# Optimization experiments

Hardware: AMD Instinct MI355X
Metric: run time of the kernel (lower is better)

Reference implementation:

```python
import jax, jax.numpy as jnp
import numpy as np

# Reconstructed from DAT's DAttentionBaseline with the wrapper's config:
# q_size=(14,14), n_heads=12, n_head_channels=64, n_groups=8, stride=1,
# offset_range_factor=1.0, use_pe=False (so log_cpb/rpe unused), no_off=False,
# ksize=3, dropout=0 (eval). Followed by the wrapper's Linear out-projection.

H = W = 14
G = 8          # n_groups
NH = 12        # n_heads
OFF_RANGE_FACTOR = 1.0


def grid_sample_bilinear(img, grid):
    # img: [B, C, H, W]; grid: [B, Hg, Wg, 2] in (x, y) order, [-1, 1],
    # align_corners=True, padding_mode='zeros' (torch defaults used by DAT).
    B, C, Hi, Wi = img.shape
    gx = (grid[..., 0] + 1.0) * 0.5 * (Wi - 1)
    gy = (grid[..., 1] + 1.0) * 0.5 * (Hi - 1)
    x0 = jnp.floor(gx)
    y0 = jnp.floor(gy)
    x1 = x0 + 1.0
    y1 = y0 + 1.0
    wx1 = gx - x0
    wx0 = 1.0 - wx1
    wy1 = gy - y0
    wy0 = 1.0 - wy1
    flat = img.reshape(B, C, Hi * Wi)

    def tap(xi, yi, wgt):
        valid = (xi >= 0) & (xi <= Wi - 1) & (yi >= 0) & (yi <= Hi - 1)
        xi_c = jnp.clip(xi, 0, Wi - 1).astype(jnp.int32)
        yi_c = jnp.clip(yi, 0, Hi - 1).astype(jnp.int32)
        idx = (yi_c * Wi + xi_c).reshape(B, 1, -1)
        vals = jnp.take_along_axis(flat, idx, axis=2)  # [B, C, Hg*Wg]
        w = (wgt * valid.astype(img.dtype)).reshape(B, 1, -1)
        return vals * w

    out = (tap(x0, y0, wx0 * wy0) + tap(x1, y0, wx1 * wy0)
           + tap(x0, y1, wx0 * wy1) + tap(x1, y1, wx1 * wy1))
    return out  # [B, C, Hg*Wg]


def setup_inputs() -> dict:
    key = jax.random.key(0)
    ks = jax.random.split(key, 16)
    B, N, C = 128, 196, 768
    Cg = C // G  # 96
    s = 0.02
    return {
        "hidden_states": jax.random.normal(ks[0], (B, N, C), jnp.float32),
        "Wq": jax.random.normal(ks[1], (C, C), jnp.float32) * s,
        "bq": jnp.zeros((C,), jnp.float32),
        "off_dw_w": jax.random.normal(ks[2], (Cg, 1, 3, 3), jnp.float32) * s,
        "off_dw_b": jnp.zeros((Cg,), jnp.float32),
        "ln_w": jnp.ones((Cg,), jnp.float32),
        "ln_b": jnp.zeros((Cg,), jnp.float32),
        "off_pw_w": jax.random.normal(ks[3], (2, Cg), jnp.float32) * s,
        "Wk": jax.random.normal(ks[4], (C, C), jnp.float32) * s,
        "bk": jnp.zeros((C,), jnp.float32),
        "Wv": jax.random.normal(ks[5], (C, C), jnp.float32) * s,
        "bv": jnp.zeros((C,), jnp.float32),
        "Wproj": jax.random.normal(ks[6], (C, C), jnp.float32) * s,
        "bproj": jnp.zeros((C,), jnp.float32),
        "Wout": jax.random.normal(ks[7], (C, C), jnp.float32) * s,
        "bout": jnp.zeros((C,), jnp.float32),
    }


def reference(hidden_states, Wq, bq, off_dw_w, off_dw_b, ln_w, ln_b, off_pw_w,
              Wk, bk, Wv, bv, Wproj, bproj, Wout, bout):
    B, N, C = hidden_states.shape
    Cg = C // G
    nh, dh = NH, C // NH
    scale = dh ** -0.5
    dt = hidden_states.dtype

    x_im = hidden_states.reshape(B, H, W, C).transpose(0, 3, 1, 2)  # [B,C,H,W]

    # proj_q: 1x1 conv
    q_im = jnp.einsum('bchw,oc->bohw', x_im, Wq) + bq[None, :, None, None]
    q_off = q_im.reshape(B * G, Cg, H, W)

    # offset net: depthwise 3x3 conv -> LayerNorm(channels) -> GELU -> 1x1 (no bias)
    t = jax.lax.conv_general_dilated(
        q_off, off_dw_w, (1, 1), [(1, 1), (1, 1)],
        dimension_numbers=('NCHW', 'OIHW', 'NCHW'), feature_group_count=Cg)
    t = t + off_dw_b[None, :, None, None]
    mu = t.mean(axis=1, keepdims=True)
    var = ((t - mu) ** 2).mean(axis=1, keepdims=True)
    t = (t - mu) * jax.lax.rsqrt(var + 1e-5)
    t = t * ln_w[None, :, None, None] + ln_b[None, :, None, None]
    t = jax.nn.gelu(t, approximate=False)
    off = jnp.einsum('bchw,oc->bohw', t, off_pw_w)  # [B*G, 2(y,x), H, W]

    off_range = jnp.array([1.0 / (H - 1), 1.0 / (W - 1)], dt).reshape(1, 2, 1, 1)
    off = jnp.tanh(off) * off_range * OFF_RANGE_FACTOR
    off = off.transpose(0, 2, 3, 1)  # [B*G, H, W, 2] (y, x)

    ry = ((jnp.arange(H, dtype=dt) + 0.5) / H) * 2.0 - 1.0
    rx = ((jnp.arange(W, dtype=dt) + 0.5) / W) * 2.0 - 1.0
    ref = jnp.stack(jnp.meshgrid(ry, rx, indexing='ij'), axis=-1)  # [H,W,2]
    pos = off + ref[None]          # (y, x)
    grid = pos[..., ::-1]          # (x, y) for grid_sample

    x_g = x_im.reshape(B * G, Cg, H, W)
    n_sample = H * W
    x_s = grid_sample_bilinear(x_g, grid).reshape(B, C, n_sample)

    k = jnp.einsum('bcn,oc->bon', x_s, Wk) + bk[None, :, None]
    v = jnp.einsum('bcn,oc->bon', x_s, Wv) + bv[None, :, None]

    qh = q_im.reshape(B, nh, dh, N)
    kh = k.reshape(B, nh, dh, n_sample)
    vh = v.reshape(B, nh, dh, n_sample)

    attn = jax.nn.softmax(jnp.einsum('bhcm,bhcn->bhmn', qh, kh) * scale, axis=-1)
    out = jnp.einsum('bhmn,bhcn->bhcm', attn, vh).reshape(B, C, N)

    y = jnp.einsum('bcn,oc->bon', out, Wproj) + bproj[None, :, None]
    y = y.transpose(0, 2, 1)               # [B, N, C]
    y = y @ Wout.T + bout                  # wrapper's Linear out-projection
    return y, attn
```

## Files before the change

### kernel.cpp

```cpp
#include <hip/hip_runtime.h>
#include <math.h>

#define Bsz 128
#define Hh 14
#define Ww 14
#define Nn 196
#define Cc 768
#define Gg 8
#define CgC 96
#define NHh 12
#define Dh 64
#define ROWS (Bsz*Nn)

typedef _Float16 half8 __attribute__((ext_vector_type(8)));
typedef _Float16 half4 __attribute__((ext_vector_type(4)));
typedef float f32x4 __attribute__((ext_vector_type(4)));

__global__ __launch_bounds__(256) void cvt_f32_f16(
    const float* __restrict__ src, _Float16* __restrict__ dst, int n8)
{
  const int i = blockIdx.x * 256 + threadIdx.x;
  if (i >= n8) return;
  float4 a = *(const float4*)(src + (size_t)i * 8);
  float4 b = *(const float4*)(src + (size_t)i * 8 + 4);
  half8 h;
  h[0]=(_Float16)a.x; h[1]=(_Float16)a.y; h[2]=(_Float16)a.z; h[3]=(_Float16)a.w;
  h[4]=(_Float16)b.x; h[5]=(_Float16)b.y; h[6]=(_Float16)b.z; h[7]=(_Float16)b.w;
  *(half8*)(dst + (size_t)i * 8) = h;
}

__global__ __launch_bounds__(256) void cvt_w5(
    const float* __restrict__ w0, const float* __restrict__ w1,
    const float* __restrict__ w2, const float* __restrict__ w3,
    const float* __restrict__ w4, _Float16* __restrict__ dst)
{
  const int i = blockIdx.x * 256 + threadIdx.x;
  const int per = Cc * Cc / 8;
  if (i >= 5 * per) return;
  const int m = i / per, r = i - m * per;
  const float* s = (m == 0) ? w0 : (m == 1) ? w1 : (m == 2) ? w2 : (m == 3) ? w3 : w4;
  float4 a = *(const float4*)(s + (size_t)r * 8);
  float4 b = *(const float4*)(s + (size_t)r * 8 + 4);
  half8 h;
  h[0]=(_Float16)a.x; h[1]=(_Float16)a.y; h[2]=(_Float16)a.z; h[3]=(_Float16)a.w;
  h[4]=(_Float16)b.x; h[5]=(_Float16)b.y; h[6]=(_Float16)b.z; h[7]=(_Float16)b.w;
  *(half8*)(dst + (size_t)m * Cc * Cc + (size_t)r * 8) = h;
}

template<int F16OUT>
__global__ __launch_bounds__(256) void gemm_h16(
    const _Float16* __restrict__ A, const _Float16* __restrict__ W,
    const float* __restrict__ bias, void* __restrict__ Cout)
{
  __shared__ __align__(16) _Float16 As[128 * 64];
  __shared__ __align__(16) _Float16 Bs[128 * 64];
  const int t = threadIdx.x;
  const int nwg = gridDim.x;
  int bid = blockIdx.x;
  bid = (bid & 7) * (nwg >> 3) + (bid >> 3);
  const int colb = bid % 6, rowb = bid / 6;
  const int row0 = rowb * 128, col0 = colb * 128;
  const int lane = t & 63, w = t >> 6;
  const int wr = w >> 1, wc = w & 1;
  const int l15 = lane & 15, l4 = lane >> 4;
  const int srow = t >> 3;
  const int sg   = t & 7;

  f32x4 acc[4][4];
#pragma unroll
  for (int i = 0; i < 4; ++i)
#pragma unroll
    for (int j = 0; j < 4; ++j) acc[i][j] = (f32x4){0.f, 0.f, 0.f, 0.f};

  for (int kt = 0; kt < 12; ++kt) {
    const int k0 = kt * 64;
#pragma unroll
    for (int it = 0; it < 4; ++it) {
      const int r = it * 32 + srow;
      half8 ha = *(const half8*)(A + (size_t)(row0 + r) * Cc + k0 + sg * 8);
      half8 hw = *(const half8*)(W + (size_t)(col0 + r) * Cc + k0 + sg * 8);
      const int dst = r * 64 + ((sg ^ (r & 7)) * 8);
      *(half8*)&As[dst] = ha;
      *(half8*)&Bs[dst] = hw;
    }
    __syncthreads();
#pragma unroll
    for (int ks = 0; ks < 2; ++ks) {
      half8 af[4], bf[4];
#pragma unroll
      for (int mi = 0; mi < 4; ++mi) {
        const int r = wr * 64 + mi * 16 + l15;
        const int g = ks * 4 + l4;
        af[mi] = *(const half8*)&As[r * 64 + ((g ^ (r & 7)) * 8)];
      }
#pragma unroll
      for (int ni = 0; ni < 4; ++ni) {
        const int r = wc * 64 + ni * 16 + l15;
        const int g = ks * 4 + l4;
        bf[ni] = *(const half8*)&Bs[r * 64 + ((g ^ (r & 7)) * 8)];
      }
#pragma unroll
      for (int mi = 0; mi < 4; ++mi)
#pragma unroll
        for (int ni = 0; ni < 4; ++ni)
          acc[mi][ni] = __builtin_amdgcn_mfma_f32_16x16x32_f16(af[mi], bf[ni], acc[mi][ni], 0, 0, 0);
    }
    __syncthreads();
  }

#pragma unroll
  for (int ni = 0; ni < 4; ++ni) {
    const int col = col0 + wc * 64 + ni * 16 + l15;
    const float bcol = bias[col];
#pragma unroll
    for (int mi = 0; mi < 4; ++mi) {
      f32x4 v = acc[mi][ni];
      const int rbase = row0 + wr * 64 + mi * 16 + l4 * 4;
#pragma unroll
      for (int r = 0; r < 4; ++r) {
        if (F16OUT) {
          ((_Float16*)Cout)[(size_t)(rbase + r) * Cc + col] = (_Float16)(v[r] + bcol);
        } else {
          ((float*)Cout)[(size_t)(rbase + r) * Cc + col] = v[r] + bcol;
        }
      }
    }
  }
}

__global__ __launch_bounds__(256) void gemm_h16_kv(
    const _Float16* __restrict__ A, const _Float16* __restrict__ Wkv,
    const float* __restrict__ bk, const float* __restrict__ bv,
    _Float16* __restrict__ K16, _Float16* __restrict__ V16)
{
  __shared__ __align__(16) _Float16 As[128 * 64];
  __shared__ __align__(16) _Float16 Bs[128 * 64];
  const int t = threadIdx.x;
  const int nwg = gridDim.x;
  int bid = blockIdx.x;
  bid = (bid & 7) * (nwg >> 3) + (bid >> 3);
  const int colb = bid % 12, rowb = bid / 12;
  const int row0 = rowb * 128, col0 = colb * 128;
  const int lane = t & 63, w = t >> 6;
  const int wr = w >> 1, wc = w & 1;
  const int l15 = lane & 15, l4 = lane >> 4;
  const int srow = t >> 3;
  const int sg   = t & 7;

  _Float16* Cout = (colb < 6) ? K16 : V16;
  const float* bias = (colb < 6) ? bk : bv;
  const int cadj = (colb < 6) ? 0 : Cc;

  f32x4 acc[4][4];
#pragma unroll
  for (int i = 0; i < 4; ++i)
#pragma unroll
    for (int j = 0; j < 4; ++j) acc[i][j] = (f32x4){0.f, 0.f, 0.f, 0.f};

  for (int kt = 0; kt < 12; ++kt) {
    const int k0 = kt * 64;
#pragma unroll
    for (int it = 0; it < 4; ++it) {
      const int r = it * 32 + srow;
      half8 ha = *(const half8*)(A + (size_t)(row0 + r) * Cc + k0 + sg * 8);
      half8 hw = *(const half8*)(Wkv + (size_t)(col0 + r) * Cc + k0 + sg * 8);
      const int dst = r * 64 + ((sg ^ (r & 7)) * 8);
      *(half8*)&As[dst] = ha;
      *(half8*)&Bs[dst] = hw;
    }
    __syncthreads();
#pragma unroll
    for (int ks = 0; ks < 2; ++ks) {
      half8 af[4], bf[4];
#pragma unroll
      for (int mi = 0; mi < 4; ++mi) {
        const int r = wr * 64 + mi * 16 + l15;
        const int g = ks * 4 + l4;
        af[mi] = *(const half8*)&As[r * 64 + ((g ^ (r & 7)) * 8)];
      }
#pragma unroll
      for (int ni = 0; ni < 4; ++ni) {
        const int r = wc * 64 + ni * 16 + l15;
        const int g = ks * 4 + l4;
        bf[ni] = *(const half8*)&Bs[r * 64 + ((g ^ (r & 7)) * 8)];
      }
#pragma unroll
      for (int mi = 0; mi < 4; ++mi)
#pragma unroll
        for (int ni = 0; ni < 4; ++ni)
          acc[mi][ni] = __builtin_amdgcn_mfma_f32_16x16x32_f16(af[mi], bf[ni], acc[mi][ni], 0, 0, 0);
    }
    __syncthreads();
  }

#pragma unroll
  for (int ni = 0; ni < 4; ++ni) {
    const int col = col0 + wc * 64 + ni * 16 + l15;
    const float bcol = bias[col - cadj];
#pragma unroll
    for (int mi = 0; mi < 4; ++mi) {
      f32x4 v = acc[mi][ni];
      const int rbase = row0 + wr * 64 + mi * 16 + l4 * 4;
#pragma unroll
      for (int r = 0; r < 4; ++r)
        Cout[(size_t)(rbase + r) * Cc + (col - cadj)] = (_Float16)(v[r] + bcol);
    }
  }
}

__global__ __launch_bounds__(512, 4) void offset_sample(
    const _Float16* __restrict__ Q16, const float* __restrict__ hidden,
    const float* __restrict__ dw_w, const float* __restrict__ dw_b,
    const float* __restrict__ ln_w, const float* __restrict__ ln_b,
    const float* __restrict__ pw_w, _Float16* __restrict__ XS)
{
  __shared__ float Qs[Nn * CgC];
  const int tid = threadIdx.x;
  const int g = blockIdx.x;
  const int b = blockIdx.y;
  const int cl = tid & 31;
  const int grp = tid >> 5;

  const size_t base = (size_t)b * Nn * Cc + g * CgC;
  for (int i = tid; i < Nn * 12; i += 512) {
    const int n = i / 12, j = i - n * 12;
    half8 hv = *(const half8*)(Q16 + base + (size_t)n * Cc + j * 8);
#pragma unroll
    for (int e = 0; e < 8; ++e) Qs[n * CgC + j * 8 + e] = (float)hv[e];
  }

  float wdw[3][9], bdw[3], wln[3], bln[3], wp0[3], wp1[3];
#pragma unroll
  for (int k = 0; k < 3; ++k) {
    const int c = cl + k * 32;
#pragma unroll
    for (int t9 = 0; t9 < 9; ++t9) wdw[k][t9] = dw_w[c * 9 + t9];
    bdw[k] = dw_b[c];
    wln[k] = ln_w[c];
    bln[k] = ln_b[c];
    wp0[k] = pw_w[c];
    wp1[k] = pw_w[CgC + c];
  }
  __syncthreads();

  const float* hb0 = hidden + base;

  for (int s0 = 0; s0 < Nn; s0 += 16) {
    const int site = s0 + grp;
    if (site >= Nn) break;
    const int h = site / Ww, w = site % Ww;

    float t[3];
#pragma unroll
    for (int k = 0; k < 3; ++k) t[k] = bdw[k];
#pragma unroll
    for (int ky = 0; ky < 3; ++ky) {
      const int hp = h + ky - 1;
      if (hp < 0 || hp > Hh - 1) continue;
#pragma unroll
      for (int kx = 0; kx < 3; ++kx) {
        const int wp = w + kx - 1;
        if (wp < 0 || wp > Ww - 1) continue;
        const float* row = &Qs[(hp * Ww + wp) * CgC + cl];
#pragma unroll
        for (int k = 0; k < 3; ++k)
          t[k] = fmaf(row[k * 32], wdw[k][ky * 3 + kx], t[k]);
      }
    }

    float s = t[0] + t[1] + t[2];
#pragma unroll
    for (int off = 1; off <= 16; off <<= 1) s += __shfl_xor(s, off, 32);
    const float mu = s * (1.f / 96.f);
    float d2 = 0.f;
#pragma unroll
    for (int k = 0; k < 3; ++k) { const float d = t[k] - mu; d2 = fmaf(d, d, d2); }
#pragma unroll
    for (int off = 1; off <= 16; off <<= 1) d2 += __shfl_xor(d2, off, 32);
    const float rstd = rsqrtf(d2 * (1.f / 96.f) + 1e-5f);

    float p0 = 0.f, p1 = 0.f;
#pragma unroll
    for (int k = 0; k < 3; ++k) {
      const float tn = (t[k] - mu) * rstd * wln[k] + bln[k];
      const float a = 0.5f * tn * (1.f + erff(tn * 0.70710678118654752f));
      p0 = fmaf(a, wp0[k], p0);
      p1 = fmaf(a, wp1[k], p1);
    }
#pragma unroll
    for (int off = 1; off <= 16; off <<= 1) {
      p0 += __shfl_xor(p0, off, 32);
      p1 += __shfl_xor(p1, off, 32);
    }

    const float offy = tanhf(p0) * (1.f / 13.f);
    const float offx = tanhf(p1) * (1.f / 13.f);
    const float refy = (h + 0.5f) / 14.f * 2.f - 1.f;
    const float refx = (w + 0.5f) / 14.f * 2.f - 1.f;
    const float gx = ((offx + refx) + 1.f) * 0.5f * 13.f;
    const float gy = ((offy + refy) + 1.f) * 0.5f * 13.f;

    const float x0f = floorf(gx), y0f = floorf(gy);
    const int x0 = (int)x0f, y0 = (int)y0f;
    const float wx1 = gx - x0f, wx0 = 1.f - wx1;
    const float wy1 = gy - y0f, wy0 = 1.f - wy1;
    const bool vx0 = (x0 >= 0) & (x0 <= 13), vx1 = (x0 + 1 >= 0) & (x0 + 1 <= 13);
    const bool vy0 = (y0 >= 0) & (y0 <= 13), vy1 = (y0 + 1 >= 0) & (y0 + 1 <= 13);
    float acc[3] = {0.f, 0.f, 0.f};
#pragma unroll
    for (int k = 0; k < 3; ++k) {
      const int c = cl + k * 32;
      if (vx0 & vy0) acc[k] = fmaf(wx0 * wy0, hb0[(size_t)(y0 * Ww + x0) * Cc + c], acc[k]);
      if (vx1 & vy0) acc[k] = fmaf(wx1 * wy0, hb0[(size_t)(y0 * Ww + x0 + 1) * Cc + c], acc[k]);
      if (vx0 & vy1) acc[k] = fmaf(wx0 * wy1, hb0[(size_t)((y0 + 1) * Ww + x0) * Cc + c], acc[k]);
      if (vx1 & vy1) acc[k] = fmaf(wx1 * wy1, hb0[(size_t)((y0 + 1) * Ww + x0 + 1) * Cc + c], acc[k]);
    }
    _Float16* xp = XS + ((size_t)b * Nn + site) * Cc + g * CgC + cl;
#pragma unroll
    for (int k = 0; k < 3; ++k) xp[k * 32] = (_Float16)acc[k];
  }
}

__global__ __launch_bounds__(512, 4) void attn_fused(
    const _Float16* __restrict__ Qm, const _Float16* __restrict__ Km,
    const _Float16* __restrict__ Vm, float* __restrict__ attn,
    _Float16* __restrict__ OUT)
{
  __shared__ __align__(16) _Float16 Kt[208 * 72];
  __shared__ __align__(16) _Float16 Vt[64 * 232];
  __shared__ __align__(16) _Float16 Ps[8][16 * 40];
  const int tid = threadIdx.x;
  const int hh = blockIdx.x, b = blockIdx.y;
  const int lane = tid & 63, wv = tid >> 6;
  const int l15 = lane & 15, l4 = lane >> 4;

  const _Float16* Qbase = Qm + (size_t)b * Nn * Cc + hh * Dh;
  const _Float16* Kbase = Km + (size_t)b * Nn * Cc + hh * Dh;
  const _Float16* Vbase = Vm + (size_t)b * Nn * Cc + hh * Dh;

  {
    const int g = tid & 7;
    for (int n = tid >> 3; n < 208; n += 64) {
      half8 hv = {};
      if (n < Nn) hv = *(const half8*)(Kbase + (size_t)n * Cc + g * 8);
      *(half8*)&Kt[n * 72 + g * 8] = hv;
    }
  }
  {
    const int d0 = (tid & 15) * 4;
    for (int n = tid >> 4; n < Nn; n += 32) {
      half4 v = *(const half4*)(Vbase + (size_t)n * Cc + d0);
      Vt[(d0 + 0) * 232 + n] = v[0];
      Vt[(d0 + 1) * 232 + n] = v[1];
      Vt[(d0 + 2) * 232 + n] = v[2];
      Vt[(d0 + 3) * 232 + n] = v[3];
    }
    for (int e = tid; e < 64 * 36; e += 512) {
      int d = e / 36, n = Nn + e % 36;
      Vt[d * 232 + n] = (_Float16)0.f;
    }
  }
  __syncthreads();

  for (int mt = wv; mt < 13; mt += 8) {
    const int qrow = mt * 16 + l15;
    const _Float16* qp = Qbase + (size_t)(qrow < Nn ? qrow : (Nn - 1)) * Cc + l4 * 8;
    half8 aq0 = *(const half8*)qp;
    half8 aq1 = *(const half8*)(qp + 32);

    f32x4 accs[13];
#pragma unroll
    for (int nt = 0; nt < 13; ++nt) accs[nt] = (f32x4){0.f, 0.f, 0.f, 0.f};
#pragma unroll
    for (int nt = 0; nt < 13; ++nt) {
      const int rb = (nt * 16 + l15) * 72;
      half8 bk0 = *(const half8*)&Kt[rb + l4 * 8];
      half8 bk1 = *(const half8*)&Kt[rb + 32 + l4 * 8];
      accs[nt] = __builtin_amdgcn_mfma_f32_16x16x32_f16(aq0, bk0, accs[nt], 0, 0, 0);
      accs[nt] = __builtin_amdgcn_mfma_f32_16x16x32_f16(aq1, bk1, accs[nt], 0, 0, 0);
    }

    float rmax[4] = {-1e30f, -1e30f, -1e30f, -1e30f};
#pragma unroll
    for (int nt = 0; nt < 13; ++nt) {
#pragma unroll
      for (int r = 0; r < 4; ++r) {
        float s = accs[nt][r] * 0.125f;
        if (nt == 12 && l15 >= 4) s = -1e30f;
        accs[nt][r] = s;
        rmax[r] = fmaxf(rmax[r], s);
      }
    }
#pragma unroll
    for (int off = 1; off <= 8; off <<= 1)
#pragma unroll
      for (int r = 0; r < 4; ++r)
        rmax[r] = fmaxf(rmax[r], __shfl_xor(rmax[r], off, 64));

    float rsum[4] = {0.f, 0.f, 0.f, 0.f};
#pragma unroll
    for (int nt = 0; nt < 13; ++nt) {
#pragma unroll
      for (int r = 0; r < 4; ++r) {
        float p = __expf(accs[nt][r] - rmax[r]);
        accs[nt][r] = p;
        rsum[r] += p;
      }
    }
#pragma unroll
    for (int off = 1; off <= 8; off <<= 1)
#pragma unroll
      for (int r = 0; r < 4; ++r)
        rsum[r] += __shfl_xor(rsum[r], off, 64);
    float rinv[4];
#pragma unroll
    for (int r = 0; r < 4; ++r) rinv[r] = 1.f / rsum[r];

    float* ab = attn + (((size_t)b * NHh + hh) * Nn) * (size_t)Nn;
#pragma unroll
    for (int nt = 0; nt < 13; ++nt) {
      const int n = nt * 16 + l15;
#pragma unroll
      for (int r = 0; r < 4; ++r) {
        float pr = accs[nt][r] * rinv[r];
        accs[nt][r] = pr;
        const int m = mt * 16 + l4 * 4 + r;
        if (m < Nn && n < Nn) ab[(size_t)m * Nn + n] = pr;
      }
    }

    f32x4 acco[4];
#pragma unroll
    for (int dt = 0; dt < 4; ++dt) acco[dt] = (f32x4){0.f, 0.f, 0.f, 0.f};
#pragma unroll
    for (int nsl = 0; nsl < 7; ++nsl) {
#pragma unroll
      for (int h2 = 0; h2 < 2; ++h2) {
        const int nt = nsl * 2 + h2;
        if (nt < 13) {
#pragma unroll
          for (int r = 0; r < 4; ++r)
            Ps[wv][(l4 * 4 + r) * 40 + h2 * 16 + l15] = (_Float16)accs[nt][r];
        } else {
#pragma unroll
          for (int r = 0; r < 4; ++r)
            Ps[wv][(l4 * 4 + r) * 40 + h2 * 16 + l15] = (_Float16)0.f;
        }
      }
      half8 ap = *(const half8*)&Ps[wv][l15 * 40 + l4 * 8];
#pragma unroll
      for (int dt = 0; dt < 4; ++dt) {
        half8 bv = *(const half8*)&Vt[(dt * 16 + l15) * 232 + nsl * 32 + l4 * 8];
        acco[dt] = __builtin_amdgcn_mfma_f32_16x16x32_f16(ap, bv, acco[dt], 0, 0, 0);
      }
    }
#pragma unroll
    for (int dt = 0; dt < 4; ++dt) {
#pragma unroll
      for (int r = 0; r < 4; ++r) {
        const int m = mt * 16 + l4 * 4 + r;
        if (m < Nn)
          OUT[((size_t)b * Nn + m) * Cc + hh * Dh + dt * 16 + l15] = (_Float16)acco[dt][r];
      }
    }
  }
}

extern "C" void kernel_launch(void* const* d_in, const int* in_sizes, int n_in,
                              void* d_out, int out_size, void* d_ws, size_t ws_size,
                              hipStream_t stream) {
  const float* hidden = (const float*)d_in[0];
  const float* Wq = (const float*)d_in[1];
  const float* bq = (const float*)d_in[2];
  const float* dw_w = (const float*)d_in[3];
  const float* dw_b = (const float*)d_in[4];
  const float* ln_w = (const float*)d_in[5];
  const float* ln_b = (const float*)d_in[6];
  const float* pw_w = (const float*)d_in[7];
  const float* Wk = (const float*)d_in[8];
  const float* bk = (const float*)d_in[9];
  const float* Wv = (const float*)d_in[10];
  const float* bv = (const float*)d_in[11];
  const float* Wp = (const float*)d_in[12];
  const float* bp = (const float*)d_in[13];
  const float* Wo = (const float*)d_in[14];
  const float* bo = (const float*)d_in[15];

  const size_t SZ = (size_t)Bsz * Nn * Cc;
  float* yout = (float*)d_out;
  float* attn = yout + SZ;

  _Float16* h16   = (_Float16*)d_ws;
  _Float16* Q16   = h16   + SZ;
  _Float16* XS16  = Q16   + SZ;
  _Float16* K16   = XS16  + SZ;
  _Float16* V16   = K16   + SZ;
  _Float16* OUT16 = V16   + SZ;
  _Float16* Y116  = OUT16 + SZ;
  _Float16* W16   = Y116  + SZ;

  const int gemm_blocks = (ROWS / 128) * (Cc / 128);
  const int kv_blocks   = (ROWS / 128) * 12;
  const int n8 = (int)(SZ / 8);

  cvt_f32_f16<<<(n8 + 255) / 256, 256, 0, stream>>>(hidden, h16, n8);
  cvt_w5<<<(5 * Cc * Cc / 8 + 255) / 256, 256, 0, stream>>>(Wq, Wk, Wv, Wp, Wo, W16);

  gemm_h16<1><<<gemm_blocks, 256, 0, stream>>>(h16, W16 + 0 * (size_t)Cc * Cc, bq, Q16);
  offset_sample<<<dim3(Gg, Bsz), 512, 0, stream>>>(Q16, hidden, dw_w, dw_b, ln_w, ln_b, pw_w, XS16);
  gemm_h16_kv<<<kv_blocks, 256, 0, stream>>>(XS16, W16 + 1 * (size_t)Cc * Cc, bk, bv, K16, V16);
  attn_fused<<<dim3(NHh, Bsz), 512, 0, stream>>>(Q16, K16, V16, attn, OUT16);
  gemm_h16<1><<<gemm_blocks, 256, 0, stream>>>(OUT16, W16 + 3 * (size_t)Cc * Cc, bp, Y116);
  gemm_h16<0><<<gemm_blocks, 256, 0, stream>>>(Y116, W16 + 4 * (size_t)Cc * Cc, bo, yout);
}
```

Before: 544.9 us.

## Fold proj and output linear layers into one precomputed weight and bias

The two back-to-back linear projections (Wproj then Wout) are merged algebraically: a small GEMM computes Wout·Wproj in fp16 and a kernel computes the fused bias Wout·bproj + bout. The activation path then runs one 25088x768x768 GEMM instead of two and no longer writes or reads the Y1 intermediate. The cost is an extra small weight GEMM per call. Rounding the fused weight to fp16 changes numerical error slightly.

```diff
diff --git a/kernel.cpp b/kernel.cpp
--- a/kernel.cpp
+++ b/kernel.cpp
@@ -45,6 +45,98 @@
   h[0]=(_Float16)a.x; h[1]=(_Float16)a.y; h[2]=(_Float16)a.z; h[3]=(_Float16)a.w;
   h[4]=(_Float16)b.x; h[5]=(_Float16)b.y; h[6]=(_Float16)b.z; h[7]=(_Float16)b.w;
   *(half8*)(dst + (size_t)m * Cc * Cc + (size_t)r * 8) = h;
+}
+
+__global__ __launch_bounds__(256) void fuse_bias(
+    const float* __restrict__ Wo, const float* __restrict__ bp,
+    const float* __restrict__ bo, float* __restrict__ bf)
+{
+  const int o2 = blockIdx.x * 256 + threadIdx.x;
+  if (o2 >= Cc) return;
+  float s = bo[o2];
+  const float* wrow = Wo + (size_t)o2 * Cc;
+  for (int o = 0; o < Cc; ++o) s = fmaf(wrow[o], bp[o], s);
+  bf[o2] = s;
+}
+
+__global__ __launch_bounds__(256) void gemm_ww(
+    const _Float16* __restrict__ Wo16, const _Float16* __restrict__ Wp16,
+    _Float16* __restrict__ Wf)
+{
+  __shared__ __align__(16) _Float16 As[128 * 64];
+  __shared__ __align__(16) _Float16 Bs[128 * 72];
+  const int t = threadIdx.x;
+  const int bid = blockIdx.x;
+  const int colb = bid % 6, rowb = bid / 6;
+  const int row0 = rowb * 128, col0 = colb * 128;
+  const int lane = t & 63, w = t >> 6;
+  const int wr = w >> 1, wc = w & 1;
+  const int l15 = lane & 15, l4 = lane >> 4;
+  const int srow = t >> 3;
+  const int sg   = t & 7;
+
+  f32x4 acc[4][4];
+#pragma unroll
+  for (int i = 0; i < 4; ++i)
+#pragma unroll
+    for (int j = 0; j < 4; ++j) acc[i][j] = (f32x4){0.f, 0.f, 0.f, 0.f};
+
+  for (int kt = 0; kt < 12; ++kt) {
+    const int k0 = kt * 64;
+#pragma unroll
+    for (int it = 0; it < 4; ++it) {
+      const int r = it * 32 + srow;
+      half8 ha = *(const half8*)(Wo16 + (size_t)(row0 + r) * Cc + k0 + sg * 8);
+      *(half8*)&As[r * 64 + ((sg ^ (r & 7)) * 8)] = ha;
+    }
+    {
+      const int og = t >> 4;
+      const int cg = t & 15;
+#pragma unroll
+      for (int it = 0; it < 4; ++it) {
+        const int o = it * 16 + og;
+        half8 hv = *(const half8*)(Wp16 + (size_t)(k0 + o) * Cc + col0 + cg * 8);
+#pragma unroll
+        for (int e = 0; e < 8; ++e)
+          Bs[(cg * 8 + e) * 72 + o] = hv[e];
+      }
+    }
+    __syncthreads();
+#pragma unroll
+    for (int ks = 0; ks < 2; ++ks) {
+      half8 af[4], bf[4];
+#pragma unroll
+      for (int mi = 0; mi < 4; ++mi) {
+        const int r = wr * 64 + mi * 16 + l15;
+        const int g = ks * 4 + l4;
+        af[mi] = *(const half8*)&As[r * 64 + ((g ^ (r & 7)) * 8)];
+      }
+#pragma unroll
+      for (int ni = 0; ni < 4; ++ni) {
+        const int c = wc * 64 + ni * 16 + l15;
+        bf[ni] = *(const half8*)&Bs[c * 72 + ks * 32 + l4 * 8];
+      }
+#pragma unroll
+      for (int mi = 0; mi < 4; ++mi)
+#pragma unroll
+        for (int ni = 0; ni < 4; ++ni)
+          acc[mi][ni] = __builtin_amdgcn_mfma_f32_16x16x32_f16(af[mi], bf[ni], acc[mi][ni], 0, 0, 0);
+    }
+    __syncthreads();
+  }
+
+#pragma unroll
+  for (int ni = 0; ni < 4; ++ni) {
+    const int col = col0 + wc * 64 + ni * 16 + l15;
+#pragma unroll
+    for (int mi = 0; mi < 4; ++mi) {
+      f32x4 v = acc[mi][ni];
+      const int rbase = row0 + wr * 64 + mi * 16 + l4 * 4;
+#pragma unroll
+      for (int r = 0; r < 4; ++r)
+        Wf[(size_t)(rbase + r) * Cc + col] = (_Float16)v[r];
+    }
+  }
 }
 
 template<int F16OUT>
@@ -496,8 +588,9 @@
   _Float16* K16   = XS16  + SZ;
   _Float16* V16   = K16   + SZ;
   _Float16* OUT16 = V16   + SZ;
-  _Float16* Y116  = OUT16 + SZ;
-  _Float16* W16   = Y116  + SZ;
+  _Float16* W16   = OUT16 + SZ;
+  _Float16* Wf16  = W16   + 5 * (size_t)Cc * Cc;
+  float*    bf    = (float*)(Wf16 + (size_t)Cc * Cc);
 
   const int gemm_blocks = (ROWS / 128) * (Cc / 128);
   const int kv_blocks   = (ROWS / 128) * 12;
@@ -505,11 +598,12 @@
 
   cvt_f32_f16<<<(n8 + 255) / 256, 256, 0, stream>>>(hidden, h16, n8);
   cvt_w5<<<(5 * Cc * Cc / 8 + 255) / 256, 256, 0, stream>>>(Wq, Wk, Wv, Wp, Wo, W16);
+  gemm_ww<<<36, 256, 0, stream>>>(W16 + 4 * (size_t)Cc * Cc, W16 + 3 * (size_t)Cc * Cc, Wf16);
+  fuse_bias<<<(Cc + 255) / 256, 256, 0, stream>>>(Wo, bp, bo, bf);
 
   gemm_h16<1><<<gemm_blocks, 256, 0, stream>>>(h16, W16 + 0 * (size_t)Cc * Cc, bq, Q16);
   offset_sample<<<dim3(Gg, Bsz), 512, 0, stream>>>(Q16, hidden, dw_w, dw_b, ln_w, ln_b, pw_w, XS16);
   gemm_h16_kv<<<kv_blocks, 256, 0, stream>>>(XS16, W16 + 1 * (size_t)Cc * Cc, bk, bv, K16, V16);
   attn_fused<<<dim3(NHh, Bsz), 512, 0, stream>>>(Q16, K16, V16, attn, OUT16);
-  gemm_h16<1><<<gemm_blocks, 256, 0, stream>>>(OUT16, W16 + 3 * (size_t)Cc * Cc, bp, Y116);
-  gemm_h16<0><<<gemm_blocks, 256, 0, stream>>>(Y116, W16 + 4 * (size_t)Cc * Cc, bo, yout);
-}
+  gemm_h16<0><<<gemm_blocks, 256, 0, stream>>>(OUT16, Wf16, bf, yout);
+}
```

Measured after the change: 548.3 us. No clear change (+0.6%).
